# Performance work log

Hardware: AMD Instinct MI355X
Metric: run time of the kernel (lower is better)

The kernel has to match this reference:

```python
import jax, jax.numpy as jnp
import numpy as np

H = 16   # num_heads
D = 16   # key_dim == output_dim (required by the module's reshape)
F = 64   # input feature dim


def setup_inputs() -> dict:
    key = jax.random.key(0)
    ks = jax.random.split(key, 8)
    B, N, Kn = 4, 4096, 32
    scale = 1.0 / np.sqrt(F)
    return {
        "inp": jax.random.normal(ks[0], (B, N, Kn, F), dtype=jnp.float32),
        "query": jax.random.normal(ks[1], (B, N, F), dtype=jnp.float32),
        "Wq": jax.random.normal(ks[2], (F, H * D), dtype=jnp.float32) * scale,
        "bq": jnp.zeros((H * D,), dtype=jnp.float32),
        "Wk": jax.random.normal(ks[3], (F, H * D), dtype=jnp.float32) * scale,
        "bk": jnp.zeros((H * D,), dtype=jnp.float32),
        "Wv": jax.random.normal(ks[4], (F, H * D), dtype=jnp.float32) * scale,
        "bv": jnp.zeros((H * D,), dtype=jnp.float32),
    }


def reference(inp, query, Wq, bq, Wk, bk, Wv, bv):
    B, N, Kn, _ = inp.shape
    # Dense projections
    Q = query @ Wq + bq                    # [B, N, H*D]
    K = inp @ Wk + bk                      # [B, N, Kn, H*D]
    V = inp @ Wv + bv                      # [B, N, Kn, H*D]
    # Faithful reshape (plain reshape of last dims, as in the TF code)
    Q = Q.reshape(B, N, H, 1, D)           # query broadcast axis of size 1
    K = K.reshape(B, N, H, Kn, D)
    V = V.reshape(B, N, H, Kn, D)
    # scaled dot-product attention per point over its Kn neighbors
    w = jnp.einsum('bnhqd,bnhkd->bnhqk', Q, K) / jnp.sqrt(jnp.float32(D))
    w = jax.nn.softmax(w, axis=-1)         # [B, N, H, 1, Kn]
    out = jnp.einsum('bnhqk,bnhkd->bnhqd', w, V)  # [B, N, H, 1, D]
    return out.reshape(B, N, H * D)
```

## Files before the change

### kernel.cpp

```cpp
#include <hip/hip_runtime.h>

#define KN 32
#define FF 64
#define CC 256
#define KV_STRIDE 260
#define VOFF (KN * KV_STRIDE)
#define NITER 16
#define QSTRIDE 264
#define WSTRIDE 33


typedef __attribute__((ext_vector_type(8)))  short bf16x8;
typedef __attribute__((ext_vector_type(16))) float f32x16;
typedef __attribute__((ext_vector_type(4)))  float f32x4;

__device__ inline unsigned short f2bf(float f) {
    union { float f; unsigned u; } v; v.f = f;
    unsigned u = v.u + 0x7fffu + ((v.u >> 16) & 1u);
    return (unsigned short)(u >> 16);
}
__device__ inline unsigned pack2(float a, float b) {
    return (unsigned)f2bf(a) | ((unsigned)f2bf(b) << 16);
}
__device__ inline bf16x8 pack8(float4 a, float4 b) {
    union { bf16x8 v; unsigned u[4]; } r;
    r.u[0] = pack2(a.x, a.y);  r.u[1] = pack2(a.z, a.w);
    r.u[2] = pack2(b.x, b.y);  r.u[3] = pack2(b.z, b.w);
    return r.v;
}

__global__ __launch_bounds__(256, 2)
void attn_one(const float* __restrict__ inp,
              const float* __restrict__ query,
              const float* __restrict__ Wq,
              const float* __restrict__ bq,
              const float* __restrict__ Wk,
              const float* __restrict__ bk,
              const float* __restrict__ Wv,
              const float* __restrict__ bv,
              float* __restrict__ out, int nPoints)
{
    __shared__ float kvS[2 * KN * KV_STRIDE];
    __shared__ unsigned short qAllS[NITER * QSTRIDE];
    __shared__ float wS[16 * WSTRIDE];

    const int tid  = threadIdx.x;
    const int wave = tid >> 6;
    const int L    = tid & 63;
    const int Lm   = L & 31;
    const int Lh   = L >> 5;
    const int h    = tid >> 4;
    const int d    = tid & 15;
    const int bid  = blockIdx.x;
    const int grid = gridDim.x;

    float* qIn = kvS;
    {
        const int i  = tid >> 4;
        const int f4 = (tid & 15) * 4;
        const int p  = bid + i * grid;
        if (p < nPoints)
            *(float4*)(qIn + i * 68 + f4) =
                *(const float4*)(query + (size_t)p * FF + f4);
    }

    float4 pf[8];
    {
        const float* arow = inp + (size_t)bid * (KN * FF) + Lm * FF + Lh * 8;
#pragma unroll
        for (int s = 0; s < 4; ++s) {
            pf[2 * s]     = *(const float4*)(arow + s * 16);
            pf[2 * s + 1] = *(const float4*)(arow + s * 16 + 4);
        }
    }

    bf16x8 Bf[4][4];
    float  bias[4];
#pragma unroll
    for (int t = 0; t < 4; ++t) {
        const float* W  = (t < 2) ? Wk : Wv;
        const float* bb = (t < 2) ? bk : bv;
        const int ch    = (2 * wave + (t & 1)) * 32 + Lm;
        bias[t] = bb[ch];
#pragma unroll
        for (int s = 0; s < 4; ++s) {
            union { bf16x8 v; unsigned u[4]; } r;
#pragma unroll
            for (int jj = 0; jj < 4; ++jj) {
                const int f = s * 16 + Lh * 8 + 2 * jj;
                r.u[jj] = pack2(W[(size_t)f * CC + ch], W[(size_t)(f + 1) * CC + ch]);
            }
            Bf[t][s] = r.v;
        }
    }

    const int nq = L & 15;
    const int kq = (L >> 4) * 8;
    bf16x8 Bq[4][2];
    float  bqv[4];
#pragma unroll
    for (int tt = 0; tt < 4; ++tt) {
        const int ch = wave * 64 + tt * 16 + nq;
        bqv[tt] = bq[ch];
#pragma unroll
        for (int s = 0; s < 2; ++s) {
            union { bf16x8 v; unsigned u[4]; } r;
#pragma unroll
            for (int jj = 0; jj < 4; ++jj) {
                const int f = s * 32 + kq + 2 * jj;
                r.u[jj] = pack2(Wq[(size_t)f * CC + ch], Wq[(size_t)(f + 1) * CC + ch]);
            }
            Bq[tt][s] = r.v;
        }
    }

    __syncthreads();

    {
        bf16x8 Aq[2];
        const int im = L & 15;
#pragma unroll
        for (int s = 0; s < 2; ++s) {
            const float* qr = qIn + im * 68 + s * 32 + kq;
            Aq[s] = pack8(*(const float4*)qr, *(const float4*)(qr + 4));
        }
#pragma unroll
        for (int tt = 0; tt < 4; ++tt) {
            f32x4 qa = {0.f, 0.f, 0.f, 0.f};
#pragma unroll
            for (int s = 0; s < 2; ++s)
                qa = __builtin_amdgcn_mfma_f32_16x16x32_bf16(Aq[s], Bq[tt][s], qa, 0, 0, 0);
            const int ch = wave * 64 + tt * 16 + nq;
#pragma unroll
            for (int r = 0; r < 4; ++r) {
                const int ip = (L >> 4) * 4 + r;
                qAllS[ip * QSTRIDE + ch] = f2bf((qa[r] + bqv[tt]) * 0.25f);
            }
        }
    }
    __syncthreads();

    for (int it = 0, p = bid; p < nPoints; ++it, p += grid) {
        bf16x8 Af[4];
#pragma unroll
        for (int s = 0; s < 4; ++s) Af[s] = pack8(pf[2 * s], pf[2 * s + 1]);

        const int pn = p + grid;
        if (pn < nPoints) {
            const float* arow = inp + (size_t)pn * (KN * FF) + Lm * FF + Lh * 8;
#pragma unroll
            for (int s = 0; s < 4; ++s) {
                pf[2 * s]     = *(const float4*)(arow + s * 16);
                pf[2 * s + 1] = *(const float4*)(arow + s * 16 + 4);
            }
        }

        f32x16 acc[4];
#pragma unroll
        for (int t = 0; t < 4; ++t)
#pragma unroll
            for (int r = 0; r < 16; ++r) acc[t][r] = 0.0f;
#pragma unroll
        for (int s = 0; s < 4; ++s)
#pragma unroll
            for (int t = 0; t < 4; ++t)
                acc[t] = __builtin_amdgcn_mfma_f32_32x32x16_bf16(Af[s], Bf[t][s], acc[t], 0, 0, 0);

#pragma unroll
        for (int t = 0; t < 4; ++t) {
            float* dstbase = kvS + ((t < 2) ? 0 : VOFF);
            const int col  = (2 * wave + (t & 1)) * 32 + Lm;
            const float bs = bias[t];
#pragma unroll
            for (int r = 0; r < 16; ++r) {
                const int jrow = (r & 3) + 8 * (r >> 2) + 4 * Lh;
                dstbase[jrow * KV_STRIDE + col] = acc[t][r] + bs;
            }
        }
        __syncthreads();

        const unsigned short* qrow = qAllS + it * QSTRIDE + h * 16;
        const int j0  = 2 * h + (d >> 3);
        const int g16 = ((2 * d) & 15) * 16;
        const float* Krow = kvS + j0 * KV_STRIDE + g16;
        float l0 = 0.f, l1 = 0.f;
#pragma unroll
        for (int i = 0; i < 16; ++i) {
            const int dp = (d + i) & 15;
            const float qv = __uint_as_float((unsigned)qrow[dp] << 16);
            l0 = fmaf(qv, Krow[dp],      l0);
            l1 = fmaf(qv, Krow[16 + dp], l1);
        }

        float m = fmaxf(l0, l1);
        m = fmaxf(m, __shfl_xor(m, 1));
        m = fmaxf(m, __shfl_xor(m, 2));
        m = fmaxf(m, __shfl_xor(m, 4));
        m = fmaxf(m, __shfl_xor(m, 8));
        float e0 = __expf(l0 - m), e1 = __expf(l1 - m);
        float s2 = e0 + e1;
        s2 += __shfl_xor(s2, 1);
        s2 += __shfl_xor(s2, 2);
        s2 += __shfl_xor(s2, 4);
        s2 += __shfl_xor(s2, 8);
        const float inv = 1.0f / s2;
        wS[h * WSTRIDE + 2 * d]     = e0 * inv;
        wS[h * WSTRIDE + 2 * d + 1] = e1 * inv;
        __builtin_amdgcn_wave_barrier();

        float o = 0.f;
        const float* Vbase = kvS + VOFF;
#pragma unroll
        for (int k = 0; k < KN; ++k) {
            const int jk = 2 * h + (k >> 4);
            o = fmaf(wS[h * WSTRIDE + k], Vbase[jk * KV_STRIDE + (k & 15) * 16 + d], o);
        }
        out[(size_t)p * CC + tid] = o;

        __syncthreads();
    }
}

extern "C" void kernel_launch(void* const* d_in, const int* in_sizes, int n_in,
                              void* d_out, int out_size, void* d_ws, size_t ws_size,
                              hipStream_t stream) {
    const float* inp   = (const float*)d_in[0];
    const float* query = (const float*)d_in[1];
    const float* Wq    = (const float*)d_in[2];
    const float* bq    = (const float*)d_in[3];
    const float* Wk    = (const float*)d_in[4];
    const float* bk    = (const float*)d_in[5];
    const float* Wv    = (const float*)d_in[6];
    const float* bv    = (const float*)d_in[7];
    float* out = (float*)d_out;

    const int nPoints = in_sizes[0] / (KN * FF);
    const int grid    = (nPoints + NITER - 1) / NITER;

    attn_one<<<grid, 256, 0, stream>>>(inp, query, Wq, bq, Wk, bk, Wv, bv,
                                       out, nPoints);
}
```

Baseline: 288.3 us.

## Store K/V tile transposed in bf16 LDS and raise occupancy to three blocks

Stores the projected K and V tile in shared memory as bf16 in a transposed, padded layout instead of fp32. This shrinks LDS use enough to allow three blocks per CU via launch bounds. The change also seeds the accumulators with the bias, uses cheaper round-up bf16 packing through a byte permute, and moves the barrier so the next prefetch happens after the LDS write. The attention dot products read packed bf16 pairs, so K and V now carry bf16 rounding error, and the round-up conversion is less exact than round-to-nearest-even.

New measurement: 641.4 us. +122.5%, slower.

```diff
diff --git a/kernel.cpp b/kernel.cpp
--- a/kernel.cpp
+++ b/kernel.cpp
@@ -3,33 +3,34 @@
 #define KN 32
 #define FF 64
 #define CC 256
-#define KV_STRIDE 260
-#define VOFF (KN * KV_STRIDE)
 #define NITER 16
-#define QSTRIDE 264
-#define WSTRIDE 33
+#define KVST 36
+#define QST 257
+#define WST 34
 
 
 typedef __attribute__((ext_vector_type(8)))  short bf16x8;
 typedef __attribute__((ext_vector_type(16))) float f32x16;
 typedef __attribute__((ext_vector_type(4)))  float f32x4;
 
-__device__ inline unsigned short f2bf(float f) {
-    union { float f; unsigned u; } v; v.f = f;
-    unsigned u = v.u + 0x7fffu + ((v.u >> 16) & 1u);
-    return (unsigned short)(u >> 16);
-}
-__device__ inline unsigned pack2(float a, float b) {
-    return (unsigned)f2bf(a) | ((unsigned)f2bf(b) << 16);
+__device__ inline unsigned pack2ru(float a, float b) {
+    unsigned au = __float_as_uint(a) + 0x8000u;
+    unsigned bu = __float_as_uint(b) + 0x8000u;
+    return __builtin_amdgcn_perm(bu, au, 0x07060302u);
+}
+__device__ inline unsigned short f2bf_ru(float a) {
+    return (unsigned short)((__float_as_uint(a) + 0x8000u) >> 16);
 }
 __device__ inline bf16x8 pack8(float4 a, float4 b) {
     union { bf16x8 v; unsigned u[4]; } r;
-    r.u[0] = pack2(a.x, a.y);  r.u[1] = pack2(a.z, a.w);
-    r.u[2] = pack2(b.x, b.y);  r.u[3] = pack2(b.z, b.w);
+    r.u[0] = pack2ru(a.x, a.y);  r.u[1] = pack2ru(a.z, a.w);
+    r.u[2] = pack2ru(b.x, b.y);  r.u[3] = pack2ru(b.z, b.w);
     return r.v;
 }
-
-__global__ __launch_bounds__(256, 2)
+__device__ inline float bflo(unsigned u) { return __uint_as_float(u << 16); }
+__device__ inline float bfhi(unsigned u) { return __uint_as_float(u & 0xffff0000u); }
+
+__global__ __launch_bounds__(256, 3)
 void attn_one(const float* __restrict__ inp,
               const float* __restrict__ query,
               const float* __restrict__ Wq,
@@ -40,9 +41,9 @@
               const float* __restrict__ bv,
               float* __restrict__ out, int nPoints)
 {
-    __shared__ float kvS[2 * KN * KV_STRIDE];
-    __shared__ unsigned short qAllS[NITER * QSTRIDE];
-    __shared__ float wS[16 * WSTRIDE];
+    __shared__ __align__(16) unsigned short kvT[512 * KVST];
+    __shared__ unsigned short qAll[NITER * QST];
+    __shared__ float wS2[16 * WST];
 
     const int tid  = threadIdx.x;
     const int wave = tid >> 6;
@@ -54,7 +55,17 @@
     const int bid  = blockIdx.x;
     const int grid = gridDim.x;
 
-    float* qIn = kvS;
+    float4 pf[8];
+    {
+        const float* arow = inp + (size_t)bid * (KN * FF) + Lm * FF + Lh * 8;
+#pragma unroll
+        for (int s = 0; s < 4; ++s) {
+            pf[2 * s]     = *(const float4*)(arow + s * 16);
+            pf[2 * s + 1] = *(const float4*)(arow + s * 16 + 4);
+        }
+    }
+
+    float* qIn = (float*)kvT;
     {
         const int i  = tid >> 4;
         const int f4 = (tid & 15) * 4;
@@ -64,16 +75,6 @@
                 *(const float4*)(query + (size_t)p * FF + f4);
     }
 
-    float4 pf[8];
-    {
-        const float* arow = inp + (size_t)bid * (KN * FF) + Lm * FF + Lh * 8;
-#pragma unroll
-        for (int s = 0; s < 4; ++s) {
-            pf[2 * s]     = *(const float4*)(arow + s * 16);
-            pf[2 * s + 1] = *(const float4*)(arow + s * 16 + 4);
-        }
-    }
-
     bf16x8 Bf[4][4];
     float  bias[4];
 #pragma unroll
@@ -88,7 +89,7 @@
 #pragma unroll
             for (int jj = 0; jj < 4; ++jj) {
                 const int f = s * 16 + Lh * 8 + 2 * jj;
-                r.u[jj] = pack2(W[(size_t)f * CC + ch], W[(size_t)(f + 1) * CC + ch]);
+                r.u[jj] = pack2ru(W[(size_t)f * CC + ch], W[(size_t)(f + 1) * CC + ch]);
             }
             Bf[t][s] = r.v;
         }
@@ -96,27 +97,26 @@
 
     const int nq = L & 15;
     const int kq = (L >> 4) * 8;
-    bf16x8 Bq[4][2];
-    float  bqv[4];
-#pragma unroll
-    for (int tt = 0; tt < 4; ++tt) {
-        const int ch = wave * 64 + tt * 16 + nq;
-        bqv[tt] = bq[ch];
-#pragma unroll
-        for (int s = 0; s < 2; ++s) {
-            union { bf16x8 v; unsigned u[4]; } r;
-#pragma unroll
-            for (int jj = 0; jj < 4; ++jj) {
-                const int f = s * 32 + kq + 2 * jj;
-                r.u[jj] = pack2(Wq[(size_t)f * CC + ch], Wq[(size_t)(f + 1) * CC + ch]);
-            }
-            Bq[tt][s] = r.v;
-        }
-    }
-
-    __syncthreads();
-
     {
+        bf16x8 Bq[4][2];
+        float  bqv[4];
+#pragma unroll
+        for (int tt = 0; tt < 4; ++tt) {
+            const int ch = wave * 64 + tt * 16 + nq;
+            bqv[tt] = bq[ch];
+#pragma unroll
+            for (int s = 0; s < 2; ++s) {
+                union { bf16x8 v; unsigned u[4]; } r;
+#pragma unroll
+                for (int jj = 0; jj < 4; ++jj) {
+                    const int f = s * 32 + kq + 2 * jj;
+                    r.u[jj] = pack2ru(Wq[(size_t)f * CC + ch], Wq[(size_t)(f + 1) * CC + ch]);
+                }
+                Bq[tt][s] = r.v;
+            }
+        }
+        __syncthreads();
+
         bf16x8 Aq[2];
         const int im = L & 15;
 #pragma unroll
@@ -134,16 +134,41 @@
 #pragma unroll
             for (int r = 0; r < 4; ++r) {
                 const int ip = (L >> 4) * 4 + r;
-                qAllS[ip * QSTRIDE + ch] = f2bf((qa[r] + bqv[tt]) * 0.25f);
-            }
-        }
-    }
-    __syncthreads();
-
-    for (int it = 0, p = bid; p < nPoints; ++it, p += grid) {
-        bf16x8 Af[4];
-#pragma unroll
-        for (int s = 0; s < 4; ++s) Af[s] = pack8(pf[2 * s], pf[2 * s + 1]);
+                qAll[ip * QST + ch] = f2bf_ru((qa[r] + bqv[tt]) * 0.25f);
+            }
+        }
+    }
+
+    for (int it = 0, p = bid; it < NITER && p < nPoints; ++it, p += grid) {
+        f32x16 acc[4];
+#pragma unroll
+        for (int t = 0; t < 4; ++t)
+#pragma unroll
+            for (int r = 0; r < 16; ++r) acc[t][r] = bias[t];
+#pragma unroll
+        for (int s = 0; s < 4; ++s) {
+            bf16x8 Af = pack8(pf[2 * s], pf[2 * s + 1]);
+#pragma unroll
+            for (int t = 0; t < 4; ++t)
+                acc[t] = __builtin_amdgcn_mfma_f32_32x32x16_bf16(Af, Bf[t][s], acc[t], 0, 0, 0);
+        }
+
+        __syncthreads();
+
+#pragma unroll
+        for (int t = 0; t < 4; ++t) {
+            const int row = ((t < 2) ? 0 : 256) + (2 * wave + (t & 1)) * 32 + Lm;
+#pragma unroll
+            for (int rg = 0; rg < 4; ++rg) {
+                const int jb = 8 * rg + 4 * Lh;
+                uint2 w2;
+                w2.x = pack2ru(acc[t][4 * rg + 0], acc[t][4 * rg + 1]);
+                w2.y = pack2ru(acc[t][4 * rg + 2], acc[t][4 * rg + 3]);
+                *(uint2*)(kvT + row * KVST + jb) = w2;
+            }
+        }
+
+        __syncthreads();
 
         const int pn = p + grid;
         if (pn < nPoints) {
@@ -155,41 +180,15 @@
             }
         }
 
-        f32x16 acc[4];
-#pragma unroll
-        for (int t = 0; t < 4; ++t)
-#pragma unroll
-            for (int r = 0; r < 16; ++r) acc[t][r] = 0.0f;
-#pragma unroll
-        for (int s = 0; s < 4; ++s)
-#pragma unroll
-            for (int t = 0; t < 4; ++t)
-                acc[t] = __builtin_amdgcn_mfma_f32_32x32x16_bf16(Af[s], Bf[t][s], acc[t], 0, 0, 0);
-
-#pragma unroll
-        for (int t = 0; t < 4; ++t) {
-            float* dstbase = kvS + ((t < 2) ? 0 : VOFF);
-            const int col  = (2 * wave + (t & 1)) * 32 + Lm;
-            const float bs = bias[t];
-#pragma unroll
-            for (int r = 0; r < 16; ++r) {
-                const int jrow = (r & 3) + 8 * (r >> 2) + 4 * Lh;
-                dstbase[jrow * KV_STRIDE + col] = acc[t][r] + bs;
-            }
-        }
-        __syncthreads();
-
-        const unsigned short* qrow = qAllS + it * QSTRIDE + h * 16;
-        const int j0  = 2 * h + (d >> 3);
-        const int g16 = ((2 * d) & 15) * 16;
-        const float* Krow = kvS + j0 * KV_STRIDE + g16;
+        const unsigned short* qrow = qAll + it * QST + h * 16;
         float l0 = 0.f, l1 = 0.f;
 #pragma unroll
         for (int i = 0; i < 16; ++i) {
             const int dp = (d + i) & 15;
-            const float qv = __uint_as_float((unsigned)qrow[dp] << 16);
-            l0 = fmaf(qv, Krow[dp],      l0);
-            l1 = fmaf(qv, Krow[16 + dp], l1);
+            const unsigned kk = *(const unsigned*)(kvT + (16 * d + dp) * KVST + 2 * h);
+            const float qv = bflo((unsigned)qrow[dp]);
+            l0 = fmaf(qv, bflo(kk), l0);
+            l1 = fmaf(qv, bfhi(kk), l1);
         }
 
         float m = fmaxf(l0, l1);
@@ -204,20 +203,18 @@
         s2 += __shfl_xor(s2, 4);
         s2 += __shfl_xor(s2, 8);
         const float inv = 1.0f / s2;
-        wS[h * WSTRIDE + 2 * d]     = e0 * inv;
-        wS[h * WSTRIDE + 2 * d + 1] = e1 * inv;
+        *(float2*)(wS2 + h * WST + 2 * d) = make_float2(e0 * inv, e1 * inv);
         __builtin_amdgcn_wave_barrier();
 
         float o = 0.f;
-        const float* Vbase = kvS + VOFF;
-#pragma unroll
-        for (int k = 0; k < KN; ++k) {
-            const int jk = 2 * h + (k >> 4);
-            o = fmaf(wS[h * WSTRIDE + k], Vbase[jk * KV_STRIDE + (k & 15) * 16 + d], o);
+#pragma unroll
+        for (int mm = 0; mm < 16; ++mm) {
+            const unsigned vv = *(const unsigned*)(kvT + (256 + 16 * mm + d) * KVST + 2 * h);
+            const float2 w = *(const float2*)(wS2 + h * WST + 2 * mm);
+            o = fmaf(w.x, bflo(vv), o);
+            o = fmaf(w.y, bfhi(vv), o);
         }
         out[(size_t)p * CC + tid] = o;
-
-        __syncthreads();
     }
 }
 
```
